# Optimization experiments

Measured on AMD Instinct MI355X. Metric: run time of the kernel, lower is better.

Reference implementation:

```python
import jax, jax.numpy as jnp
import numpy as np

H, W, F = 64, 64, 64  # ca_shape and inner_filters
N = H * W  # flattened attention length

def conv2d_same(x, Wt, b):
    # x: [B,H,W,Cin], Wt: [kh,kw,Cin,Cout] (HWIO)
    y = jax.lax.conv_general_dilated(x, Wt, window_strides=(1, 1), padding='SAME',
                                     dimension_numbers=('NHWC', 'HWIO', 'NHWC'))
    return y + b

def setup_inputs() -> dict:
    key = jax.random.key(0)
    ks = jax.random.split(key, 9)
    s = 0.05  # small init scale to keep softmax logits sane
    return {
        'x':  jax.random.normal(ks[0], (4, H, W, 64), jnp.float32),
        'Wk': jax.random.normal(ks[1], (3, 3, 64, F), jnp.float32) * s,
        'bk': jnp.zeros((F,), jnp.float32),
        'Wq': jax.random.normal(ks[2], (3, 3, 64, F), jnp.float32) * s,
        'bq': jnp.zeros((F,), jnp.float32),
        'Wv': jax.random.normal(ks[3], (3, 3, 64, F), jnp.float32) * s,
        'bv': jnp.zeros((F,), jnp.float32),
        'Wr': jax.random.normal(ks[4], (3, 3, F, 64), jnp.float32) * s,
        'br': jnp.zeros((64,), jnp.float32),
    }

def reference(x, Wk, bk, Wq, bq, Wv, bv, Wr, br):
    B = x.shape[0]
    k = jax.nn.elu(conv2d_same(x, Wk, bk)).reshape(B, N, F)
    q = jax.nn.elu(conv2d_same(x, Wq, bq)).reshape(B, N, F)
    v = jax.nn.relu(conv2d_same(x, Wv, bv)).reshape(B, N, F)
    # QK^T with diagonal zeroed (multiplied by 1 - I, NOT -inf), then scaled
    scores = jnp.einsum('bnf,bmf->bnm', q, k)
    mask = 1.0 - jnp.eye(N, dtype=scores.dtype)  # broadcast over batch
    scores = scores * mask / jnp.sqrt(jnp.asarray(F, scores.dtype))
    attn = jax.nn.softmax(scores, axis=-1)
    out = jnp.einsum('bnm,bmf->bnf', attn, v).reshape(B, H, W, F)
    return jax.nn.relu(conv2d_same(out, Wr, br))
```

## Files before the change

kernel.cpp:

```cpp
#include <hip/hip_runtime.h>
#include <hip/hip_bf16.h>
#include <math.h>

#define B_ 4
#define H_ 64
#define W_ 64
#define C_ 64
#define F_ 64
#define N_ 4096

typedef __attribute__((ext_vector_type(8))) short bf16x8;
typedef __attribute__((ext_vector_type(4))) short bf16x4;
typedef __attribute__((ext_vector_type(4))) float f32x4;
typedef __attribute__((ext_vector_type(2))) int i32x2;

static __device__ __forceinline__ short f2bf(float f){
  union { __hip_bfloat16 h; short s; } u;
  u.h = __float2bfloat16(f);
  return u.s;
}

__global__ __launch_bounds__(256) void prep_x_kernel(
    const float* __restrict__ x, short* __restrict__ xb)
{
  const int i4 = blockIdx.x * 256 + threadIdx.x;
  const float4 v = ((const float4*)x)[i4];
  bf16x4 o;
  o[0] = f2bf(v.x); o[1] = f2bf(v.y); o[2] = f2bf(v.z); o[3] = f2bf(v.w);
  ((bf16x4*)xb)[i4] = o;
}

__global__ __launch_bounds__(256) void prep_w_kernel(
    const float* __restrict__ Wk, const float* __restrict__ Wq,
    const float* __restrict__ Wv, const float* __restrict__ Wr,
    short* __restrict__ Wt)
{
  const int gid = blockIdx.x * 256 + threadIdx.x;
  const int oc = gid / 576;
  const int kk = gid % 576;
  const int srcofs = (kk >> 6) * 4096 + (kk & 63) * 64 + (oc & 63);
  const float* src = (oc < 64) ? Wk : (oc < 128) ? Wq : (oc < 192) ? Wv : Wr;
  Wt[gid] = f2bf(src[srcofs]);
}

__global__ __launch_bounds__(256) void conv_qkv_mfma(
    const short* __restrict__ xb, const short* __restrict__ Wt,
    const float* __restrict__ bk, const float* __restrict__ bq,
    const float* __restrict__ bv,
    short* __restrict__ qo, short* __restrict__ ko, short* __restrict__ vt)
{
  const int lane = threadIdx.x & 63;
  const int w    = threadIdx.x >> 6;
  const int lrow = lane & 15;
  const int lkb  = lane >> 4;
  const int p0   = blockIdx.x << 5;
  const int b    = p0 >> 12;
  const int y    = (p0 >> 6) & 63;
  const int x0   = p0 & 63;

  f32x4 ak[2], aq[2], av[2];
  #pragma unroll
  for (int m = 0; m < 2; ++m)
    #pragma unroll
    for (int i = 0; i < 4; ++i){ ak[m][i] = 0.f; aq[m][i] = 0.f; av[m][i] = 0.f; }

  const short* wr_k = Wt + (      w * 16 + lrow) * 576;
  const short* wr_q = Wt + ( 64 + w * 16 + lrow) * 576;
  const short* wr_v = Wt + (128 + w * 16 + lrow) * 576;

  #pragma unroll
  for (int ks = 0; ks < 18; ++ks){
    const int kxy = ks >> 1;
    const int ky  = kxy / 3;
    const int kx  = kxy - ky * 3;
    const int ci0 = (ks & 1) << 5;
    const int yy  = y + ky - 1;
    const bf16x8 wk8 = *(const bf16x8*)(wr_k + ks * 32 + lkb * 8);
    const bf16x8 wq8 = *(const bf16x8*)(wr_q + ks * 32 + lkb * 8);
    const bf16x8 wv8 = *(const bf16x8*)(wr_v + ks * 32 + lkb * 8);
    #pragma unroll
    for (int m = 0; m < 2; ++m){
      const int xx = x0 + m * 16 + lrow + kx - 1;
      bf16x8 a = {0,0,0,0,0,0,0,0};
      if ((unsigned)yy < 64u && (unsigned)xx < 64u)
        a = *(const bf16x8*)(xb + ((((b << 6) + yy) << 6) + xx) * 64 + ci0 + lkb * 8);
      ak[m] = __builtin_amdgcn_mfma_f32_16x16x32_bf16(a, wk8, ak[m], 0, 0, 0);
      aq[m] = __builtin_amdgcn_mfma_f32_16x16x32_bf16(a, wq8, aq[m], 0, 0, 0);
      av[m] = __builtin_amdgcn_mfma_f32_16x16x32_bf16(a, wv8, av[m], 0, 0, 0);
    }
  }
  const int oc = w * 16 + lrow;
  const float bkv = bk[oc], bqv = bq[oc], bvv = bv[oc];
  #pragma unroll
  for (int m = 0; m < 2; ++m){
    bf16x4 vp;
    #pragma unroll
    for (int i = 0; i < 4; ++i){
      const int p = p0 + m * 16 + (lkb << 2) + i;
      const float kvv = ak[m][i] + bkv;
      ko[p * 64 + oc] = f2bf(kvv > 0.f ? kvv : expm1f(kvv));
      const float qvv = aq[m][i] + bqv;
      const float qe  = (qvv > 0.f ? qvv : expm1f(qvv)) * 0.125f;
      qo[p * 64 + oc] = f2bf(qe);
      const float vvv = av[m][i] + bvv;
      vp[i] = f2bf(vvv > 0.f ? vvv : 0.f);
    }
    *(bf16x4*)(vt + ((size_t)(b * 64 + oc)) * 4096 + (p0 & 4095) + m * 16 + (lkb << 2)) = vp;
  }
}

__global__ __launch_bounds__(256, 3) void attn_kernel(
    const short* __restrict__ q, const short* __restrict__ k,
    const short* __restrict__ vt, float* __restrict__ Op,
    float* __restrict__ lp, int split)
{
  const int tid  = threadIdx.x;
  const int lane = tid & 63;
  const int wv   = tid >> 6;
  const int lrow = lane & 15;
  const int lkb  = lane >> 4;

  const int bid  = blockIdx.x;
  const int b    = bid / (32 * split);
  const int rem  = bid % (32 * split);
  const int rt   = rem / split;
  const int sp   = rem % split;
  const int rbase = (rt << 7) + (wv << 5);
  const int tiles = (N_ / 64) / split;
  const int ct0   = sp * tiles;

  const short* qb = q  + (size_t)b * N_ * F_;
  const short* kb = k  + (size_t)b * N_ * F_;
  const short* vb = vt + (size_t)b * F_ * N_;

  const bf16x8 aq00 = *(const bf16x8*)(qb + (rbase +      lrow) * F_ + lkb * 8);
  const bf16x8 aq01 = *(const bf16x8*)(qb + (rbase +      lrow) * F_ + 32 + lkb * 8);
  const bf16x8 aq10 = *(const bf16x8*)(qb + (rbase + 16 + lrow) * F_ + lkb * 8);
  const bf16x8 aq11 = *(const bf16x8*)(qb + (rbase + 16 + lrow) * F_ + 32 + lkb * 8);

  __shared__ short kbuf[2][64 * 64];
  __shared__ short vbuf[2][64 * 64];
  __shared__ short pbuf[4][2][16][64];

  const int srow = tid >> 3;
  const int sc16 = tid & 7;
  const int dst0 = (srow * 128)        + ((sc16 * 16) ^ ((srow & 7) << 4));
  const int dst1 = ((srow + 32) * 128) + ((sc16 * 16) ^ ((srow & 7) << 4));

  f32x4 oacc[2][4];
  float l_r[2] = {0.f, 0.f};
  #pragma unroll
  for (int g = 0; g < 2; ++g)
    #pragma unroll
    for (int fs = 0; fs < 4; ++fs)
      #pragma unroll
      for (int i = 0; i < 4; ++i) oacc[g][fs][i] = 0.f;

  int cbase = ct0 << 6;
  bf16x8 sk0 = *(const bf16x8*)(kb + (cbase + srow) * 64      + sc16 * 8);
  bf16x8 sk1 = *(const bf16x8*)(kb + (cbase + srow + 32) * 64 + sc16 * 8);
  bf16x8 sv0 = *(const bf16x8*)(vb + (size_t)srow * N_        + cbase + sc16 * 8);
  bf16x8 sv1 = *(const bf16x8*)(vb + (size_t)(srow + 32) * N_ + cbase + sc16 * 8);
  *(bf16x8*)((char*)kbuf[0] + dst0) = sk0;
  *(bf16x8*)((char*)kbuf[0] + dst1) = sk1;
  *(bf16x8*)((char*)vbuf[0] + dst0) = sv0;
  *(bf16x8*)((char*)vbuf[0] + dst1) = sv1;
  __syncthreads();

  int cur = 0;
  for (int t = 0; t < tiles; ++t){
    cbase = (ct0 + t) << 6;
    if (t + 1 < tiles){
      const int cb2 = (ct0 + t + 1) << 6;
      sk0 = *(const bf16x8*)(kb + (cb2 + srow) * 64      + sc16 * 8);
      sk1 = *(const bf16x8*)(kb + (cb2 + srow + 32) * 64 + sc16 * 8);
      sv0 = *(const bf16x8*)(vb + (size_t)srow * N_        + cb2 + sc16 * 8);
      sv1 = *(const bf16x8*)(vb + (size_t)(srow + 32) * N_ + cb2 + sc16 * 8);
    }
    const char* kc = (const char*)kbuf[cur];
    const char* vc = (const char*)vbuf[cur];
    f32x4 s0[4], s1[4];
    #pragma unroll
    for (int n = 0; n < 4; ++n){
      #pragma unroll
      for (int i = 0; i < 4; ++i){ s0[n][i] = 0.f; s1[n][i] = 0.f; }
    }
    #pragma unroll
    for (int n = 0; n < 4; ++n){
      const int r   = n * 16 + lrow;
      const int swz = (r & 7) << 4;
      const bf16x8 b0 = *(const bf16x8*)(kc + r * 128 + ((lkb * 16) ^ swz));
      const bf16x8 b1 = *(const bf16x8*)(kc + r * 128 + ((64 + lkb * 16) ^ swz));
      s0[n] = __builtin_amdgcn_mfma_f32_16x16x32_bf16(b0, aq00, s0[n], 0, 0, 0);
      s0[n] = __builtin_amdgcn_mfma_f32_16x16x32_bf16(b1, aq01, s0[n], 0, 0, 0);
      s1[n] = __builtin_amdgcn_mfma_f32_16x16x32_bf16(b0, aq10, s1[n], 0, 0, 0);
      s1[n] = __builtin_amdgcn_mfma_f32_16x16x32_bf16(b1, aq11, s1[n], 0, 0, 0);
    }
    const int rswz = (lrow & 7) << 4;
    #pragma unroll
    for (int g = 0; g < 2; ++g){
      f32x4* s = g ? s1 : s0;
      const int dq = rbase + g * 16 - cbase;
      if (dq >= 0 && dq < 64){
        #pragma unroll
        for (int n = 0; n < 4; ++n)
          if (dq == n * 16){
            const int di = lrow - (lkb << 2);
            #pragma unroll
            for (int i = 0; i < 4; ++i)
              if (di == i) s[n][i] = 0.f;
          }
      }
      char* pgc = (char*)&pbuf[wv][g][0][0];
      #pragma unroll
      for (int n = 0; n < 4; ++n){
        union { float f; unsigned u; } c0, c1, c2, c3;
        c0.f = __expf(s[n][0] - 16.f);
        c1.f = __expf(s[n][1] - 16.f);
        c2.f = __expf(s[n][2] - 16.f);
        c3.f = __expf(s[n][3] - 16.f);
        l_r[g] += (c0.f + c1.f) + (c2.f + c3.f);
        i32x2 pk;
        pk[0] = (int)((c1.u & 0xFFFF0000u) | (c0.u >> 16));
        pk[1] = (int)((c3.u & 0xFFFF0000u) | (c2.u >> 16));
        *(i32x2*)(pgc + lrow * 128 + ((n * 32 + lkb * 8) ^ rswz)) = pk;
      }
      const bf16x8 pa0 = *(const bf16x8*)(pgc + lrow * 128 + ((lkb * 16) ^ rswz));
      const bf16x8 pa1 = *(const bf16x8*)(pgc + lrow * 128 + ((64 + lkb * 16) ^ rswz));
      #pragma unroll
      for (int kc2 = 0; kc2 < 2; ++kc2){
        const bf16x8 pa = kc2 ? pa1 : pa0;
        #pragma unroll
        for (int fs = 0; fs < 4; ++fs){
          const int r   = fs * 16 + lrow;
          const int swz = (r & 7) << 4;
          const bf16x8 bvf = *(const bf16x8*)(vc + r * 128 + ((kc2 * 64 + lkb * 16) ^ swz));
          oacc[g][fs] = __builtin_amdgcn_mfma_f32_16x16x32_bf16(pa, bvf, oacc[g][fs], 0, 0, 0);
        }
      }
    }
    if (t + 1 < tiles){
      const int nxt = cur ^ 1;
      *(bf16x8*)((char*)kbuf[nxt] + dst0) = sk0;
      *(bf16x8*)((char*)kbuf[nxt] + dst1) = sk1;
      *(bf16x8*)((char*)vbuf[nxt] + dst0) = sv0;
      *(bf16x8*)((char*)vbuf[nxt] + dst1) = sv1;
    }
    __syncthreads();
    cur ^= 1;
  }
  #pragma unroll
  for (int g = 0; g < 2; ++g){
    l_r[g] += __shfl_xor(l_r[g], 16, 64);
    l_r[g] += __shfl_xor(l_r[g], 32, 64);
  }
  float* Ob = Op + (size_t)(b * split + sp) * N_ * F_;
  #pragma unroll
  for (int g = 0; g < 2; ++g){
    #pragma unroll
    for (int i = 0; i < 4; ++i){
      const int row = rbase + g * 16 + lkb * 4 + i;
      #pragma unroll
      for (int fs = 0; fs < 4; ++fs)
        Ob[(size_t)row * F_ + fs * 16 + lrow] = oacc[g][fs][i];
    }
    if (lane < 16)
      lp[(size_t)(b * split + sp) * N_ + rbase + g * 16 + lane] = l_r[g];
  }
}

__global__ __launch_bounds__(256) void combine_kernel(
    const float* __restrict__ Op, const float* __restrict__ lp,
    short* __restrict__ ob, int split)
{
  const int gid = blockIdx.x * 256 + threadIdx.x;
  const int f = gid & 63;
  const int n = (gid >> 6) & (N_ - 1);
  const int b = gid >> 18;
  float L = 0.f, O = 0.f;
  for (int s = 0; s < split; ++s){
    L += lp[(size_t)(b * split + s) * N_ + n];
    O += Op[((size_t)(b * split + s) * N_ + n) * F_ + f];
  }
  ob[gid] = f2bf(O / L);
}

__global__ __launch_bounds__(256) void conv_out_mfma(
    const short* __restrict__ ab, const short* __restrict__ Wt,
    const float* __restrict__ br, float* __restrict__ out)
{
  const int lane = threadIdx.x & 63;
  const int w    = threadIdx.x >> 6;
  const int lrow = lane & 15;
  const int lkb  = lane >> 4;
  const int p0   = blockIdx.x << 5;
  const int b    = p0 >> 12;
  const int y    = (p0 >> 6) & 63;
  const int x0   = p0 & 63;

  f32x4 acc[2];
  #pragma unroll
  for (int m = 0; m < 2; ++m)
    #pragma unroll
    for (int i = 0; i < 4; ++i) acc[m][i] = 0.f;
  const short* wr = Wt + (192 + w * 16 + lrow) * 576;

  #pragma unroll
  for (int ks = 0; ks < 18; ++ks){
    const int kxy = ks >> 1;
    const int ky  = kxy / 3;
    const int kx  = kxy - ky * 3;
    const int ci0 = (ks & 1) << 5;
    const int yy  = y + ky - 1;
    const bf16x8 w8 = *(const bf16x8*)(wr + ks * 32 + lkb * 8);
    #pragma unroll
    for (int m = 0; m < 2; ++m){
      const int xx = x0 + m * 16 + lrow + kx - 1;
      bf16x8 a = {0,0,0,0,0,0,0,0};
      if ((unsigned)yy < 64u && (unsigned)xx < 64u)
        a = *(const bf16x8*)(ab + ((((b << 6) + yy) << 6) + xx) * 64 + ci0 + lkb * 8);
      acc[m] = __builtin_amdgcn_mfma_f32_16x16x32_bf16(a, w8, acc[m], 0, 0, 0);
    }
  }
  const int oc = w * 16 + lrow;
  const float bb = br[oc];
  #pragma unroll
  for (int m = 0; m < 2; ++m)
    #pragma unroll
    for (int i = 0; i < 4; ++i){
      const int p = p0 + m * 16 + (lkb << 2) + i;
      out[(size_t)p * 64 + oc] = fmaxf(acc[m][i] + bb, 0.f);
    }
}

extern "C" void kernel_launch(void* const* d_in, const int* in_sizes, int n_in,
                              void* d_out, int out_size, void* d_ws, size_t ws_size,
                              hipStream_t stream)
{
  const float* x  = (const float*)d_in[0];
  const float* Wk = (const float*)d_in[1];
  const float* bk = (const float*)d_in[2];
  const float* Wq = (const float*)d_in[3];
  const float* bq = (const float*)d_in[4];
  const float* Wv = (const float*)d_in[5];
  const float* bv = (const float*)d_in[6];
  const float* Wr = (const float*)d_in[7];
  const float* br = (const float*)d_in[8];
  float* out = (float*)d_out;

  const size_t BNF = (size_t)B_ * N_ * F_;
  const size_t fixed_shorts = BNF * 5 + 256 * 576;
  const size_t fixed_bytes  = fixed_shorts * 2;
  int split = 8;
  while (split > 1 &&
         fixed_bytes + (size_t)split * (BNF * 4 + (size_t)B_ * N_ * 4) > ws_size)
    split >>= 1;

  short* xb16 = (short*)d_ws;
  short* Wt   = xb16 + BNF;
  short* qw   = Wt + 256 * 576;
  short* kw   = qw + BNF;
  short* vt   = kw + BNF;
  short* attnb= vt + BNF;
  float* Op   = (float*)(attnb + BNF);
  float* lp   = Op + (size_t)split * BNF;

  hipLaunchKernelGGL(prep_x_kernel, dim3(1024), dim3(256), 0, stream, x, xb16);
  hipLaunchKernelGGL(prep_w_kernel, dim3(576), dim3(256), 0, stream, Wk, Wq, Wv, Wr, Wt);
  hipLaunchKernelGGL(conv_qkv_mfma, dim3(512), dim3(256), 0, stream,
                     xb16, Wt, bk, bq, bv, qw, kw, vt);
  hipLaunchKernelGGL(attn_kernel, dim3(B_ * 32 * split), dim3(256), 0, stream,
                     qw, kw, vt, Op, lp, split);
  hipLaunchKernelGGL(combine_kernel, dim3((B_ * N_ * F_) / 256), dim3(256), 0, stream,
                     Op, lp, attnb, split);
  hipLaunchKernelGGL(conv_out_mfma, dim3(512), dim3(256), 0, stream,
                     attnb, Wt, br, out);
}
```

Measured before the change: 91.39 us.

## Widen attention blocks to 512 threads, fuse prep kernels, vectorize combine

The attention kernel now uses 8 waves per block covering 256 query rows. Each K/V tile staged in shared memory is shared by twice as many rows, and each thread loads one 16-byte chunk instead of two. The two prep kernels are merged into one launch, and the combine kernel handles four features per thread with float4 loads and a reciprocal multiply. The aims are to cut global K/V traffic per query row and to trim launch and memory overhead. The risk is that the grid has half as many blocks and larger blocks may lower occupancy.

```diff
diff --git a/kernel.cpp b/kernel.cpp
--- a/kernel.cpp
+++ b/kernel.cpp
@@ -20,27 +20,27 @@
   return u.s;
 }
 
-__global__ __launch_bounds__(256) void prep_x_kernel(
-    const float* __restrict__ x, short* __restrict__ xb)
-{
-  const int i4 = blockIdx.x * 256 + threadIdx.x;
-  const float4 v = ((const float4*)x)[i4];
-  bf16x4 o;
-  o[0] = f2bf(v.x); o[1] = f2bf(v.y); o[2] = f2bf(v.z); o[3] = f2bf(v.w);
-  ((bf16x4*)xb)[i4] = o;
-}
-
-__global__ __launch_bounds__(256) void prep_w_kernel(
+__global__ __launch_bounds__(256) void prep_kernel(
+    const float* __restrict__ x,
     const float* __restrict__ Wk, const float* __restrict__ Wq,
     const float* __restrict__ Wv, const float* __restrict__ Wr,
-    short* __restrict__ Wt)
-{
-  const int gid = blockIdx.x * 256 + threadIdx.x;
-  const int oc = gid / 576;
-  const int kk = gid % 576;
-  const int srcofs = (kk >> 6) * 4096 + (kk & 63) * 64 + (oc & 63);
-  const float* src = (oc < 64) ? Wk : (oc < 128) ? Wq : (oc < 192) ? Wv : Wr;
-  Wt[gid] = f2bf(src[srcofs]);
+    short* __restrict__ xb, short* __restrict__ Wt)
+{
+  const int bid = blockIdx.x;
+  if (bid < 1024){
+    const int i4 = bid * 256 + threadIdx.x;
+    const float4 v = ((const float4*)x)[i4];
+    bf16x4 o;
+    o[0] = f2bf(v.x); o[1] = f2bf(v.y); o[2] = f2bf(v.z); o[3] = f2bf(v.w);
+    ((bf16x4*)xb)[i4] = o;
+  } else {
+    const int gid = (bid - 1024) * 256 + threadIdx.x;
+    const int oc = gid / 576;
+    const int kk = gid % 576;
+    const int srcofs = (kk >> 6) * 4096 + (kk & 63) * 64 + (oc & 63);
+    const float* src = (oc < 64) ? Wk : (oc < 128) ? Wq : (oc < 192) ? Wv : Wr;
+    Wt[gid] = f2bf(src[srcofs]);
+  }
 }
 
 __global__ __launch_bounds__(256) void conv_qkv_mfma(
@@ -109,7 +109,7 @@
   }
 }
 
-__global__ __launch_bounds__(256, 3) void attn_kernel(
+__global__ __launch_bounds__(512, 4) void attn_kernel(
     const short* __restrict__ q, const short* __restrict__ k,
     const short* __restrict__ vt, float* __restrict__ Op,
     float* __restrict__ lp, int split)
@@ -121,11 +121,11 @@
   const int lkb  = lane >> 4;
 
   const int bid  = blockIdx.x;
-  const int b    = bid / (32 * split);
-  const int rem  = bid % (32 * split);
+  const int b    = bid / (16 * split);
+  const int rem  = bid % (16 * split);
   const int rt   = rem / split;
   const int sp   = rem % split;
-  const int rbase = (rt << 7) + (wv << 5);
+  const int rbase = (rt << 8) + (wv << 5);
   const int tiles = (N_ / 64) / split;
   const int ct0   = sp * tiles;
 
@@ -140,12 +140,11 @@
 
   __shared__ short kbuf[2][64 * 64];
   __shared__ short vbuf[2][64 * 64];
-  __shared__ short pbuf[4][2][16][64];
+  __shared__ short pbuf[8][2][16][64];
 
   const int srow = tid >> 3;
   const int sc16 = tid & 7;
-  const int dst0 = (srow * 128)        + ((sc16 * 16) ^ ((srow & 7) << 4));
-  const int dst1 = ((srow + 32) * 128) + ((sc16 * 16) ^ ((srow & 7) << 4));
+  const int dst  = (srow * 128) + ((sc16 * 16) ^ ((srow & 7) << 4));
 
   f32x4 oacc[2][4];
   float l_r[2] = {0.f, 0.f};
@@ -157,14 +156,10 @@
       for (int i = 0; i < 4; ++i) oacc[g][fs][i] = 0.f;
 
   int cbase = ct0 << 6;
-  bf16x8 sk0 = *(const bf16x8*)(kb + (cbase + srow) * 64      + sc16 * 8);
-  bf16x8 sk1 = *(const bf16x8*)(kb + (cbase + srow + 32) * 64 + sc16 * 8);
-  bf16x8 sv0 = *(const bf16x8*)(vb + (size_t)srow * N_        + cbase + sc16 * 8);
-  bf16x8 sv1 = *(const bf16x8*)(vb + (size_t)(srow + 32) * N_ + cbase + sc16 * 8);
-  *(bf16x8*)((char*)kbuf[0] + dst0) = sk0;
-  *(bf16x8*)((char*)kbuf[0] + dst1) = sk1;
-  *(bf16x8*)((char*)vbuf[0] + dst0) = sv0;
-  *(bf16x8*)((char*)vbuf[0] + dst1) = sv1;
+  bf16x8 sk = *(const bf16x8*)(kb + (cbase + srow) * 64 + sc16 * 8);
+  bf16x8 sv = *(const bf16x8*)(vb + (size_t)srow * N_ + cbase + sc16 * 8);
+  *(bf16x8*)((char*)kbuf[0] + dst) = sk;
+  *(bf16x8*)((char*)vbuf[0] + dst) = sv;
   __syncthreads();
 
   int cur = 0;
@@ -172,10 +167,8 @@
     cbase = (ct0 + t) << 6;
     if (t + 1 < tiles){
       const int cb2 = (ct0 + t + 1) << 6;
-      sk0 = *(const bf16x8*)(kb + (cb2 + srow) * 64      + sc16 * 8);
-      sk1 = *(const bf16x8*)(kb + (cb2 + srow + 32) * 64 + sc16 * 8);
-      sv0 = *(const bf16x8*)(vb + (size_t)srow * N_        + cb2 + sc16 * 8);
-      sv1 = *(const bf16x8*)(vb + (size_t)(srow + 32) * N_ + cb2 + sc16 * 8);
+      sk = *(const bf16x8*)(kb + (cb2 + srow) * 64 + sc16 * 8);
+      sv = *(const bf16x8*)(vb + (size_t)srow * N_ + cb2 + sc16 * 8);
     }
     const char* kc = (const char*)kbuf[cur];
     const char* vc = (const char*)vbuf[cur];
@@ -241,10 +234,8 @@
     }
     if (t + 1 < tiles){
       const int nxt = cur ^ 1;
-      *(bf16x8*)((char*)kbuf[nxt] + dst0) = sk0;
-      *(bf16x8*)((char*)kbuf[nxt] + dst1) = sk1;
-      *(bf16x8*)((char*)vbuf[nxt] + dst0) = sv0;
-      *(bf16x8*)((char*)vbuf[nxt] + dst1) = sv1;
+      *(bf16x8*)((char*)kbuf[nxt] + dst) = sk;
+      *(bf16x8*)((char*)vbuf[nxt] + dst) = sv;
     }
     __syncthreads();
     cur ^= 1;
@@ -273,16 +264,22 @@
     const float* __restrict__ Op, const float* __restrict__ lp,
     short* __restrict__ ob, int split)
 {
-  const int gid = blockIdx.x * 256 + threadIdx.x;
-  const int f = gid & 63;
-  const int n = (gid >> 6) & (N_ - 1);
-  const int b = gid >> 18;
-  float L = 0.f, O = 0.f;
+  const int gid4 = blockIdx.x * 256 + threadIdx.x;
+  const int f4 = gid4 & 15;
+  const int n  = (gid4 >> 4) & (N_ - 1);
+  const int b  = gid4 >> 16;
+  float L = 0.f;
+  float4 O = {0.f, 0.f, 0.f, 0.f};
   for (int s = 0; s < split; ++s){
     L += lp[(size_t)(b * split + s) * N_ + n];
-    O += Op[((size_t)(b * split + s) * N_ + n) * F_ + f];
-  }
-  ob[gid] = f2bf(O / L);
+    const float4 v = *(const float4*)(Op + (((size_t)(b * split + s) * N_ + n) << 6) + f4 * 4);
+    O.x += v.x; O.y += v.y; O.z += v.z; O.w += v.w;
+  }
+  const float inv = 1.f / L;
+  bf16x4 o;
+  o[0] = f2bf(O.x * inv); o[1] = f2bf(O.y * inv);
+  o[2] = f2bf(O.z * inv); o[3] = f2bf(O.w * inv);
+  *(bf16x4*)(ob + (size_t)gid4 * 4) = o;
 }
 
 __global__ __launch_bounds__(256) void conv_out_mfma(
@@ -365,13 +362,13 @@
   float* Op   = (float*)(attnb + BNF);
   float* lp   = Op + (size_t)split * BNF;
 
-  hipLaunchKernelGGL(prep_x_kernel, dim3(1024), dim3(256), 0, stream, x, xb16);
-  hipLaunchKernelGGL(prep_w_kernel, dim3(576), dim3(256), 0, stream, Wk, Wq, Wv, Wr, Wt);
+  hipLaunchKernelGGL(prep_kernel, dim3(1600), dim3(256), 0, stream,
+                     x, Wk, Wq, Wv, Wr, xb16, Wt);
   hipLaunchKernelGGL(conv_qkv_mfma, dim3(512), dim3(256), 0, stream,
                      xb16, Wt, bk, bq, bv, qw, kw, vt);
-  hipLaunchKernelGGL(attn_kernel, dim3(B_ * 32 * split), dim3(256), 0, stream,
+  hipLaunchKernelGGL(attn_kernel, dim3(B_ * 16 * split), dim3(512), 0, stream,
                      qw, kw, vt, Op, lp, split);
-  hipLaunchKernelGGL(combine_kernel, dim3((B_ * N_ * F_) / 256), dim3(256), 0, stream,
+  hipLaunchKernelGGL(combine_kernel, dim3((B_ * N_ * F_) / 1024), dim3(256), 0, stream,
                      Op, lp, attnb, split);
   hipLaunchKernelGGL(conv_out_mfma, dim3(512), dim3(256), 0, stream,
                      attnb, Wt, br, out);
```

New measurement: 84.11 us. 8.0% less time.
